# Performance work log

Measured on AMD Instinct MI355X. Metric: run time of the kernel, lower is better.

## Reference

```python
import jax, jax.numpy as jnp
import numpy as np
from jax import lax

FH, FW = 14, 14
HID = 1024

def _coord():
    idx = np.arange(FH * FW)
    c = np.stack([(idx / FW - FH // 2) / (FH / 2.0), (idx % FW - FW // 2) / (FW / 2.0)], axis=1)
    # view(1,H,W,2) -> transpose(2,3) -> transpose(1,2) == (1,2,H,W)
    return jnp.asarray(c.reshape(1, FH, FW, 2).transpose(0, 3, 1, 2), jnp.float32)

def _l2n(x, axis):
    # F.normalize: x / max(||x||_2, 1e-12)
    return x / jnp.maximum(jnp.linalg.norm(x, axis=axis, keepdims=True), 1e-12)

def _conv(x, w, b, pad):
    y = lax.conv_general_dilated(x, w, (1, 1), [(pad, pad), (pad, pad)],
                                 dimension_numbers=('NCHW', 'OIHW', 'NCHW'))
    return y + b[None, :, None, None]

def _bn(x, g, b):
    # BatchNorm2d in training mode: batch statistics, eps=1e-5
    m = jnp.mean(x, (0, 2, 3), keepdims=True)
    v = jnp.var(x, (0, 2, 3), keepdims=True)
    return g[None, :, None, None] * (x - m) * lax.rsqrt(v + 1e-5) + b[None, :, None, None]

def _lstm(x, w_ih, w_hh, b_ih, b_hh):
    # x: [S,B,E]; PyTorch gate order i,f,g,o
    B = x.shape[1]
    h0 = jnp.zeros((B, HID), x.dtype)
    def step(carry, xt):
        h, c = carry
        g = xt @ w_ih.T + h @ w_hh.T + (b_ih + b_hh)
        i, f, gg, o = jnp.split(g, 4, axis=-1)
        c = jax.nn.sigmoid(f) * c + jax.nn.sigmoid(i) * jnp.tanh(gg)
        h = jax.nn.sigmoid(o) * jnp.tanh(c)
        return (h, c), h
    _, hs = lax.scan(step, (h0, h0), x)
    return hs  # [S,B,HID]

def _res(v, coord, c1w, c1b, c2w, c2b, g, b):
    v = jnp.concatenate([v, coord], 1)            # [B,130,14,14]
    v1 = jax.nn.relu(_conv(v, c1w, c1b, 0))        # 1x1 conv
    v2 = jax.nn.relu(_bn(_conv(v1, c2w, c2b, 1), g, b))
    return v2 + v1

def _forward(que, img, emb_table, w_ih_f, w_hh_f, b_ih_f, b_hh_f, w_ih_b, w_hh_b, b_ih_b, b_hh_b,
             conv_w, conv_b, bn_g, bn_b, r1c1_w, r1c1_b, r1c2_w, r1c2_b, r1bn_g, r1bn_b,
             r2c1_w, r2c1_b, r2c2_w, r2c2_b, r2bn_g, r2bn_b):
    emb_table = emb_table.at[0].set(0.0)  # padding_idx=0
    x = jnp.swapaxes(emb_table[que], 0, 1)                 # [S,B,300]
    hf = _lstm(x, w_ih_f, w_hh_f, b_ih_f, b_hh_f)
    hb = _lstm(x[::-1], w_ih_b, w_hh_b, b_ih_b, b_hh_b)[::-1]
    qenc = _l2n(jnp.concatenate([hf, hb], -1), -1)         # [S,B,2048]
    enc = qenc[-1]                                         # [B,2048]
    v = _l2n(img, 1)                                       # L2 norm over channels per pixel
    B = img.shape[0]
    coord = jnp.broadcast_to(_coord(), (B, 2, FH, FW))
    v = jnp.concatenate([v, coord], 1)                     # [B,1026,14,14]
    v = jax.nn.relu(_bn(_conv(v, conv_w, conv_b, 1), bn_g, bn_b))
    v = _res(v, coord, r1c1_w, r1c1_b, r1c2_w, r1c2_b, r1bn_g, r1bn_b)
    v = _res(v, coord, r2c1_w, r2c1_b, r2c2_w, r2c2_b, r2bn_g, r2bn_b)
    return enc, qenc, v

def setup_inputs():
    key = jax.random.key(0)
    ks = jax.random.split(key, 32)
    B, S, V = 128, 32, 10000
    def n(k, shape, s=0.03):
        return jax.random.normal(k, shape, jnp.float32) * s
    return {
        'que': jax.random.randint(ks[0], (B, S), 0, V + 1),
        'img': jax.random.normal(ks[1], (B, 1024, FH, FW), jnp.float32),
        'emb_table': n(ks[2], (V + 1, 300), 0.1),
        'w_ih_f': n(ks[3], (4 * HID, 300)), 'w_hh_f': n(ks[4], (4 * HID, HID)),
        'b_ih_f': n(ks[5], (4 * HID,)), 'b_hh_f': n(ks[6], (4 * HID,)),
        'w_ih_b': n(ks[7], (4 * HID, 300)), 'w_hh_b': n(ks[8], (4 * HID, HID)),
        'b_ih_b': n(ks[9], (4 * HID,)), 'b_hh_b': n(ks[10], (4 * HID,)),
        'conv_w': n(ks[11], (128, 1026, 3, 3)), 'conv_b': n(ks[12], (128,)),
        'bn_g': jnp.ones((128,), jnp.float32), 'bn_b': jnp.zeros((128,), jnp.float32),
        'r1c1_w': n(ks[13], (128, 130, 1, 1)), 'r1c1_b': n(ks[14], (128,)),
        'r1c2_w': n(ks[15], (128, 128, 3, 3)), 'r1c2_b': n(ks[16], (128,)),
        'r1bn_g': jnp.ones((128,), jnp.float32), 'r1bn_b': jnp.zeros((128,), jnp.float32),
        'r2c1_w': n(ks[17], (128, 130, 1, 1)), 'r2c1_b': n(ks[18], (128,)),
        'r2c2_w': n(ks[19], (128, 128, 3, 3)), 'r2c2_b': n(ks[20], (128,)),
        'r2bn_g': jnp.ones((128,), jnp.float32), 'r2bn_b': jnp.zeros((128,), jnp.float32),
    }

def reference(que, img, emb_table, w_ih_f, w_hh_f, b_ih_f, b_hh_f, w_ih_b, w_hh_b, b_ih_b, b_hh_b,
              conv_w, conv_b, bn_g, bn_b, r1c1_w, r1c1_b, r1c2_w, r1c2_b, r1bn_g, r1bn_b,
              r2c1_w, r2c1_b, r2c2_w, r2c2_b, r2bn_g, r2bn_b):
    return _forward(que, img, emb_table, w_ih_f, w_hh_f, b_ih_f, b_hh_f, w_ih_b, w_hh_b, b_ih_b, b_hh_b,
                    conv_w, conv_b, bn_g, bn_b, r1c1_w, r1c1_b, r1c2_w, r1c2_b, r1bn_g, r1bn_b,
                    r2c1_w, r2c1_b, r2c2_w, r2c2_b, r2bn_g, r2bn_b)
```

## Files before the change

### kernel.cpp

```cpp
#include <hip/hip_runtime.h>
#include <hip/hip_bf16.h>
#include <math.h>


namespace {

constexpr int S_ = 32, B_ = 128, H_ = 1024, P_ = 196, OC_ = 128;
constexpr int NE = B_ * OC_ * P_;
constexpr int KC = 44;

typedef __attribute__((ext_vector_type(8))) short short8v;
typedef __attribute__((ext_vector_type(4))) short short4v;
typedef __attribute__((ext_vector_type(4))) float f32x4;
#define MFMA16(a, b, c) __builtin_amdgcn_mfma_f32_16x16x32_bf16((a), (b), (c), 0, 0, 0)

__device__ __forceinline__ float sigm(float x){ return 1.0f/(1.0f + expf(-x)); }
__device__ __forceinline__ float c0f(int p){ return ((float)p/14.0f - 7.0f)/7.0f; }
__device__ __forceinline__ float c1f(int p){ return ((float)(p%14) - 7.0f)/7.0f; }
__device__ __forceinline__ unsigned short f2bf(float x){
  __hip_bfloat16 h = __float2bfloat16(x);
  return *reinterpret_cast<unsigned short*>(&h);
}
__device__ __forceinline__ float bf2f(unsigned short u){
  unsigned v = ((unsigned)u) << 16;
  union { unsigned u; float f; } c; c.u = v; return c.f;
}

__global__ void k_packW2(const float* __restrict__ wihf, const float* __restrict__ whhf,
                         const float* __restrict__ wihb, const float* __restrict__ whhb,
                         unsigned short* __restrict__ pk){
  int i = blockIdx.x*256 + threadIdx.x;
  if (i >= 2*32*4*2*KC*64) return;
  const int lane = i & 63;
  int t = i >> 6;
  const int kc = t % KC; t /= KC;
  const int pair = t % 2; t /= 2;
  const int w = t % 4; t /= 4;
  const int uslab = t % 32; t /= 32;
  const int dir = t;
  const int lr = lane & 15, lk = lane >> 4;
  const int row = (pair*2 + (lr >> 3))*1024 + uslab*32 + w*8 + (lr & 7);
  unsigned short v[8];
  if (kc < 12){
    const float* src = dir ? wihb : wihf;
    #pragma unroll
    for (int j = 0; j < 8; ++j){
      int k = kc*32 + lk*8 + j;
      v[j] = (k < 300) ? f2bf(src[(size_t)row*300 + k]) : (unsigned short)0;
    }
  } else {
    const float* src = dir ? whhb : whhf;
    #pragma unroll
    for (int j = 0; j < 8; ++j)
      v[j] = f2bf(src[(size_t)row*1024 + (kc-12)*32 + lk*8 + j]);
  }
  unsigned short* dst = pk + (size_t)i*8;
  #pragma unroll
  for (int j = 0; j < 8; ++j) dst[j] = v[j];
}

__global__ void k_embed_px(const int* __restrict__ que, const float* __restrict__ emb,
                           unsigned short* __restrict__ px){
  int i = blockIdx.x*256 + threadIdx.x;
  if (i >= 32*8*12*64) return;
  const int lane = i & 63;
  int t2 = i >> 6;
  const int kc = t2 % 12; t2 /= 12;
  const int mgrp = t2 % 8; t2 /= 8;
  const int t = t2;
  const int b = mgrp*16 + (lane & 15);
  const int tok = que[b*S_ + t];
  const int k0 = kc*32 + (lane >> 4)*8;
  unsigned short* dst = px + (size_t)i*8;
  #pragma unroll
  for (int j = 0; j < 8; ++j){
    int k = k0 + j;
    dst[j] = (tok == 0 || k >= 300) ? (unsigned short)0 : f2bf(emb[(size_t)tok*300 + k]);
  }
}

__launch_bounds__(256, 4)
__global__ void k_xg(const unsigned short* __restrict__ px,
                     const unsigned short* __restrict__ pkW2,
                     unsigned short* __restrict__ xg){
  const int dir = blockIdx.x >> 5, uslab = blockIdx.x & 31;
  const int mslab = blockIdx.y;
  const int xs = blockIdx.z;
  const int tid = threadIdx.x, w = tid >> 6, lane = tid & 63;

  const unsigned short* pb = pkW2 + ((((size_t)(dir*32 + uslab)*4 + w)*2)*KC*64 + lane)*8;
  const size_t pbPair = (size_t)KC*512;
  const unsigned short* pax = px + (((size_t)(xs*8 + mslab*2)*12)*64 + lane)*8;
  const size_t paxRf = (size_t)12*512;

  f32x4 a00{0,0,0,0}, a01{0,0,0,0}, a10{0,0,0,0}, a11{0,0,0,0};
  #pragma unroll 4
  for (int ch = 0; ch < 12; ++ch){
    short8v a0 = *(const short8v*)(pax + (size_t)ch*512);
    short8v a1 = *(const short8v*)(pax + paxRf + (size_t)ch*512);
    short8v b0 = *(const short8v*)(pb + (size_t)ch*512);
    short8v b1 = *(const short8v*)(pb + pbPair + (size_t)ch*512);
    a00 = MFMA16(a0, b0, a00); a01 = MFMA16(a0, b1, a01);
    a10 = MFMA16(a1, b0, a10); a11 = MFMA16(a1, b1, a11);
  }

  const size_t rid = (((size_t)((xs*2 + dir)*4 + mslab)*32 + uslab)*4 + w);
  unsigned short* rec = xg + rid*1024;
  f32x4 accs[4] = {a00, a01, a10, a11};
  #pragma unroll
  for (int r = 0; r < 2; ++r)
    #pragma unroll
    for (int p = 0; p < 2; ++p){
      f32x4 v = accs[r*2 + p];
      short4v sv;
      #pragma unroll
      for (int j = 0; j < 4; ++j) sv[j] = (short)f2bf(v[j]);
      *(short4v*)(rec + ((p*2 + r)*64 + lane)*4) = sv;
    }
}

__global__ void k_packC(const float* __restrict__ w, unsigned short* __restrict__ pk,
                        int cin, int T){
  int i = blockIdx.x*256 + threadIdx.x;
  if (i >= 9*8*T*64) return;
  const int lane = i & 63;
  int t = i >> 6;
  const int kc = t % T; t /= T;
  const int ot = t % 8; t /= 8;
  const int s = t;
  const int oc = ot*16 + (lane & 15);
  const int c0 = kc*32 + (lane >> 4)*8;
  unsigned short* dst = pk + (((size_t)(s*8 + ot)*T + kc)*64 + lane)*8;
  #pragma unroll
  for (int j = 0; j < 8; ++j){
    int c = c0 + j;
    dst[j] = (c < cin) ? f2bf(w[((size_t)oc*cin + c)*9 + s]) : (unsigned short)0;
  }
}

__global__ void k_packG(const float* __restrict__ w, unsigned short* __restrict__ pk,
                        int cin, int T){
  int i = blockIdx.x*256 + threadIdx.x;
  if (i >= 8*T*64) return;
  const int lane = i & 63;
  int t = i >> 6;
  const int kc = t % T; t /= T;
  const int ot = t;
  const int oc = ot*16 + (lane & 15);
  const int c0 = kc*32 + (lane >> 4)*8;
  unsigned short* dst = pk + (((size_t)(ot*T + kc))*64 + lane)*8;
  #pragma unroll
  for (int j = 0; j < 8; ++j){
    int c = c0 + j;
    dst[j] = (c < cin) ? f2bf(w[(size_t)oc*cin + c]) : (unsigned short)0;
  }
}

__global__ void k_bias2(const float* __restrict__ bif, const float* __restrict__ bhf,
                        const float* __restrict__ bib, const float* __restrict__ bhb,
                        float* __restrict__ out){
  int i = blockIdx.x*256 + threadIdx.x;
  if (i >= 8192) return;
  out[i] = (i < 4096) ? (bif[i] + bhf[i]) : (bib[i-4096] + bhb[i-4096]);
}

__global__ void k_coordT(unsigned short* __restrict__ outT){
  int i = blockIdx.x*256 + threadIdx.x;
  if (i >= 128*196*32) return;
  int c2 = i & 31; int t = i >> 5; int p = t % 196; int b = t / 196;
  float v = (c2 == 0) ? c0f(p) : (c2 == 1) ? c1f(p) : 0.f;
  outT[((size_t)b*196 + p)*160 + 128 + c2] = f2bf(v);
}

__launch_bounds__(256, 2)
__global__ void k_step10(const unsigned short* __restrict__ xg,
                         const unsigned short* __restrict__ pkW2,
                         const float* __restrict__ bias2,
                         const unsigned short* __restrict__ hin,
                         unsigned short* __restrict__ hout,
                         float* __restrict__ cst, float* __restrict__ Q, int s){
  const int dir   = blockIdx.x >> 5;
  const int uslab = blockIdx.x & 31;
  const int mslab = blockIdx.y;
  const int m0g   = mslab*32;
  const int tid = threadIdx.x, w = tid >> 6, lane = tid & 63;
  const int lr = lane & 15, lk = lane >> 4;
  const int xs = dir ? (S_-1-s) : s;

  __shared__ unsigned short tA[32][1032];

  {
    const int r = tid >> 3, sg = tid & 7;
    const unsigned short* hr = hin + ((size_t)dir*B_ + m0g + r)*H_ + sg*128;
    #pragma unroll
    for (int q = 0; q < 16; ++q)
      *(short8v*)&tA[r][sg*128 + q*8] = *(const short8v*)(hr + q*8);
  }

  const size_t rid = (((size_t)((xs*2 + dir)*4 + mslab)*32 + uslab)*4 + w);
  const unsigned short* rec = xg + rid*1024;
  f32x4 a00, a01, a10, a11;
  {
    short4v s00 = *(const short4v*)(rec + ((0*2 + 0)*64 + lane)*4);
    short4v s01 = *(const short4v*)(rec + ((1*2 + 0)*64 + lane)*4);
    short4v s10 = *(const short4v*)(rec + ((0*2 + 1)*64 + lane)*4);
    short4v s11 = *(const short4v*)(rec + ((1*2 + 1)*64 + lane)*4);
    #pragma unroll
    for (int j = 0; j < 4; ++j){
      a00[j] = bf2f((unsigned short)s00[j]);
      a01[j] = bf2f((unsigned short)s01[j]);
      a10[j] = bf2f((unsigned short)s10[j]);
      a11[j] = bf2f((unsigned short)s11[j]);
    }
  }

  const unsigned short* pb = pkW2 + ((((size_t)(dir*32 + uslab)*4 + w)*2)*KC*64 + lane)*8;
  const size_t pbPair = (size_t)KC*512;

  __syncthreads();

  #pragma unroll 8
  for (int ch = 0; ch < 32; ++ch){
    const int ka = ch*32 + lk*8;
    short8v a0 = *(short8v*)&tA[lr][ka];
    short8v a1 = *(short8v*)&tA[16 + lr][ka];
    short8v b0 = *(const short8v*)(pb + (size_t)(12 + ch)*512);
    short8v b1 = *(const short8v*)(pb + pbPair + (size_t)(12 + ch)*512);
    a00 = MFMA16(a0, b0, a00); a01 = MFMA16(a0, b1, a01);
    a10 = MFMA16(a1, b0, a10); a11 = MFMA16(a1, b1, a11);
  }

  const int ug = uslab*32 + w*8 + (lr & 7);
  const float* bb = bias2 + (size_t)dir*4096;
  const float bi = bb[ug], bfv = bb[1024+ug], bg = bb[2048+ug], bo = bb[3072+ug];
  float* cc = cst + (size_t)dir*B_*H_;
  unsigned short* ho = hout + (size_t)dir*B_*H_;
  const int jbase = (lr & 8) ? 2 : 0;

  #pragma unroll
  for (int rf = 0; rf < 2; ++rf){
    f32x4 c0 = rf ? a10 : a00;
    f32x4 c1 = rf ? a11 : a01;
    float p0[4], p1[4];
    #pragma unroll
    for (int j = 0; j < 4; ++j){
      p0[j] = __shfl_xor(c0[j], 8, 64);
      p1[j] = __shfl_xor(c1[j], 8, 64);
    }
    #pragma unroll
    for (int q = 0; q < 2; ++q){
      const int jj = jbase + q;
      float gi, gf, gg, go;
      if (lr & 8){ gi = p0[jj]; gf = c0[jj]; gg = p1[jj]; go = c1[jj]; }
      else       { gi = c0[jj]; gf = p0[jj]; gg = c1[jj]; go = p1[jj]; }
      gi += bi; gf += bfv; gg += bg; go += bo;
      const int m = m0g + rf*16 + lk*4 + jj;
      const size_t coff = (size_t)m*H_ + ug;
      float cold = cc[coff];
      float cn = sigm(gf)*cold + sigm(gi)*tanhf(gg);
      float hn = sigm(go)*tanhf(cn);
      cc[coff] = cn;
      ho[coff] = f2bf(hn);
      Q[((size_t)xs*B_ + m)*2048 + dir*1024 + ug] = hn;
    }
  }
}

__global__ void k_qnorm(float* __restrict__ Q, float* __restrict__ enc){
  int sb = blockIdx.x;
  int s = sb >> 7, b = sb & 127;
  float* row = Q + (size_t)sb*2048;
  int tid = threadIdx.x;
  float v[8]; float ss = 0.f;
  #pragma unroll
  for (int i = 0; i < 8; ++i){ v[i] = row[tid*8+i]; ss += v[i]*v[i]; }
  __shared__ float red[256];
  red[tid] = ss; __syncthreads();
  for (int st = 128; st; st >>= 1){
    if (tid < st) red[tid] += red[tid+st];
    __syncthreads();
  }
  float inv = 1.0f / fmaxf(sqrtf(red[0]), 1e-12f);
  #pragma unroll
  for (int i = 0; i < 8; ++i){
    float q = v[i]*inv;
    row[tid*8+i] = q;
    if (s == S_-1) enc[(size_t)b*2048 + tid*8 + i] = q;
  }
}

__global__ void k_sqpart(const float* __restrict__ img, float* __restrict__ part){
  int b = blockIdx.x, cq = blockIdx.y;
  int t = threadIdx.x;
  if (t >= P_) return;
  const float* base = img + ((size_t)b*1024 + cq*256)*P_ + t;
  float s = 0.f;
  #pragma unroll 4
  for (int c = 0; c < 256; ++c){ float v = base[c*P_]; s += v*v; }
  part[((size_t)b*4 + cq)*P_ + t] = s;
}

__global__ void k_invnorm(const float* __restrict__ part, float* __restrict__ inv){
  int i = blockIdx.x*256 + threadIdx.x;
  if (i >= B_*P_) return;
  int b = i / P_, p = i % P_;
  float s = part[(b*4+0)*P_+p] + part[(b*4+1)*P_+p]
          + part[(b*4+2)*P_+p] + part[(b*4+3)*P_+p];
  inv[i] = 1.0f / fmaxf(sqrtf(s), 1e-12f);
}

__global__ void k_mkimgT(const float* __restrict__ img, const float* __restrict__ invn,
                         unsigned short* __restrict__ imgT){
  const int b = blockIdx.x, cg = blockIdx.y;
  const int tid = threadIdx.x;
  unsigned short* dstB = imgT + (size_t)b*196*1056;
  if (cg == 8){
    for (int i = tid; i < 196*32; i += 256){
      int p = i >> 5, cc = i & 31;
      float v = (cc == 0) ? c0f(p) : (cc == 1) ? c1f(p) : 0.f;
      dstB[(size_t)p*1056 + 1024 + cc] = f2bf(v);
    }
    return;
  }
  __shared__ unsigned short tt[196][136];
  __shared__ float sInv[200];
  for (int i = tid; i < 196; i += 256) sInv[i] = invn[b*196 + i];
  __syncthreads();
  const int c0 = cg*128;
  const float* srcB = img + ((size_t)b*1024 + c0)*196;
  for (int i = tid; i < 128*49; i += 256){
    int c = i / 49, p4 = i - (i/49)*49;
    float4 v = *(const float4*)(srcB + (size_t)c*196 + p4*4);
    int p = p4*4;
    tt[p+0][c] = f2bf(v.x * sInv[p+0]);
    tt[p+1][c] = f2bf(v.y * sInv[p+1]);
    tt[p+2][c] = f2bf(v.z * sInv[p+2]);
    tt[p+3][c] = f2bf(v.w * sInv[p+3]);
  }
  __syncthreads();
  for (int i = tid; i < 196*16; i += 256){
    int p = i >> 4, g = i & 15;
    *(short8v*)(dstB + (size_t)p*1056 + c0 + g*8) = *(short8v*)&tt[p][g*8];
  }
}

template<int CPAD>
__device__ __forceinline__ void stage3t(unsigned short (*__restrict__ tile)[40],
                                        const unsigned short* __restrict__ src,
                                        int c0, int r0, int tid){
  for (int i = tid; i < 10*14*4; i += 256){
    int t = i / 56, rem = i - t*56, gx = rem >> 2, seg = rem & 3;
    int gy = r0 - 1 + t;
    if ((unsigned)gy < 14u){
      short8v v = *(const short8v*)(src + (size_t)(gy*14+gx)*CPAD + c0 + seg*8);
      *(short8v*)&tile[t*16 + gx + 1][seg*8] = v;
    }
  }
}

template<int CPAD>
__launch_bounds__(256, 2)
__global__ void k_conv3t(const unsigned short* __restrict__ srcT,
                         const unsigned short* __restrict__ wPk,
                         const float* __restrict__ bias,
                         float* __restrict__ out){
  constexpr int T = CPAD / 32;
  const int b = blockIdx.x, n = blockIdx.y, z = blockIdx.z;
  const int r0 = n ? 6 : 0;
  const int chBeg = z ? T/2 : 0, chEnd = z ? T : T/2;
  const int tid = threadIdx.x, wave = tid >> 6, lane = tid & 63;
  const int lr = lane & 15, lk = lane >> 4;
  const int wfM = wave >> 1, wfN = wave & 1;
  const unsigned short* src = srcT + (size_t)b*196*CPAD;

  __shared__ unsigned short tile[2][164][40];

  for (int i = tid; i < 1640; i += 256)
    ((short8v*)&tile[0][0][0])[i] = short8v{0,0,0,0,0,0,0,0};
  __syncthreads();
  stage3t<CPAD>(tile[0], src, chBeg*32, r0, tid);
  __syncthreads();

  f32x4 acc[4][4];
  #pragma unroll
  for (int i = 0; i < 4; ++i)
    #pragma unroll
    for (int j = 0; j < 4; ++j) acc[i][j] = f32x4{0,0,0,0};

  short8v aC[12], aN[12];
  #pragma unroll
  for (int dx = 0; dx < 3; ++dx)
    #pragma unroll
    for (int rf = 0; rf < 4; ++rf)
      aC[dx*4+rf] = *(const short8v*)(wPk + ((((size_t)dx*8 + wfM*4 + rf)*T + chBeg)*64
                                             + lane)*8);

  for (int ch = chBeg; ch < chEnd; ++ch){
    const int cur = (ch - chBeg) & 1;
    #pragma unroll
    for (int dy = 0; dy < 3; ++dy){
      const int ndy = (dy < 2) ? dy + 1 : 0;
      const int nch = (dy < 2) ? ch : ch + 1;
      const bool hasN = nch < chEnd;
      if (hasN){
        #pragma unroll
        for (int dx = 0; dx < 3; ++dx)
          #pragma unroll
          for (int rf = 0; rf < 4; ++rf)
            aN[dx*4+rf] = *(const short8v*)(wPk + ((((size_t)(ndy*3+dx)*8 + wfM*4 + rf)*T
                                                    + nch)*64 + lane)*8);
      }
      #pragma unroll
      for (int dx = 0; dx < 3; ++dx){
        const int dlt = dy*16 + dx;
        #pragma unroll
        for (int cf = 0; cf < 4; ++cf){
          short8v bf = *(short8v*)&tile[cur][wfN*64 + cf*16 + lr + dlt][lk*8];
          #pragma unroll
          for (int rf = 0; rf < 4; ++rf)
            acc[rf][cf] = MFMA16(aC[dx*4+rf], bf, acc[rf][cf]);
        }
      }
      if (dy == 0 && ch + 1 < chEnd)
        stage3t<CPAD>(tile[cur^1], src, (ch+1)*32, r0, tid);
      if (hasN){
        #pragma unroll
        for (int q = 0; q < 12; ++q) aC[q] = aN[q];
      }
    }
    __syncthreads();
  }

  #pragma unroll
  for (int rf = 0; rf < 4; ++rf){
    #pragma unroll
    for (int j = 0; j < 4; ++j){
      const int oc = wfM*64 + rf*16 + lk*4 + j;
      const float bz = z ? 0.f : bias[oc];
      #pragma unroll
      for (int cf = 0; cf < 4; ++cf){
        const int pos = wfN*64 + cf*16 + lr;
        const int py = r0 + (pos >> 4), px = pos & 15;
        const bool rowok = n ? (py >= 8) : true;
        if (rowok && px < 14)
          out[(size_t)z*NE + ((size_t)b*OC_ + oc)*P_ + py*14 + px] = acc[rf][cf][j] + bz;
      }
    }
  }
}

__global__ void k_bnstats2(const float* __restrict__ t, float* __restrict__ bpart){
  const int o = blockIdx.x, part = blockIdx.y;
  const int tid = threadIdx.x;
  float s = 0.f, s2 = 0.f;
  for (int i = tid; i < 16*196; i += 256){
    int b = part*16 + i/196, p = i - (i/196)*196;
    size_t off = ((size_t)b*OC_ + o)*P_ + p;
    float v = t[off] + t[off + NE];
    s += v; s2 += v*v;
  }
  __shared__ float r1[256], r2[256];
  r1[tid] = s; r2[tid] = s2; __syncthreads();
  for (int st = 128; st; st >>= 1){
    if (tid < st){ r1[tid] += r1[tid+st]; r2[tid] += r2[tid+st]; }
    __syncthreads();
  }
  if (tid == 0){
    bpart[(o*8 + part)*2]     = r1[0];
    bpart[(o*8 + part)*2 + 1] = r2[0];
  }
}

__global__ void k_bnfin(const float* __restrict__ bpart, float* __restrict__ stats){
  int o = threadIdx.x;
  if (o >= 128) return;
  float s = 0.f, s2 = 0.f;
  #pragma unroll
  for (int q = 0; q < 8; ++q){
    s  += bpart[(o*8 + q)*2];
    s2 += bpart[(o*8 + q)*2 + 1];
  }
  float n = (float)(B_*P_);
  float m = s / n;
  float var = s2 / n - m*m;
  stats[o*2]   = m;
  stats[o*2+1] = rsqrtf(var + 1e-5f);
}

template<bool ADD, bool FINAL>
__global__ void k_bntr(const float* __restrict__ t, const float* __restrict__ stats,
                       const float* __restrict__ g, const float* __restrict__ bb,
                       const float* __restrict__ addsrc,
                       float* __restrict__ outF, unsigned short* __restrict__ outT){
  const int b = blockIdx.x, seg = blockIdx.y, tid = threadIdx.x;
  for (int i = tid; i < 16*196; i += 256){
    int c = seg*16 + i/196, p = i - (i/196)*196;
    size_t off = ((size_t)b*OC_ + c)*P_ + p;
    float x = t[off] + t[off + NE];
    float v = g[c]*(x - stats[c*2])*stats[c*2+1] + bb[c];
    v = fmaxf(v, 0.f);
    if (ADD) v += addsrc[off];
    if (FINAL) outF[off] = v;
    else       outT[((size_t)b*P_ + p)*160 + c] = f2bf(v);
  }
}

__launch_bounds__(256, 2)
__global__ void k_c1m(const unsigned short* __restrict__ vT,
                      const unsigned short* __restrict__ pk,
                      const float* __restrict__ bias,
                      float* __restrict__ out, unsigned short* __restrict__ outT){
  const int b = blockIdx.x, n = blockIdx.y;
  const int pBeg = n ? 112 : 0;
  const int nCF = n ? 6 : 7;
  const int tid = threadIdx.x, wave = tid >> 6, lane = tid & 63;
  const int lr = lane & 15, lk = lane >> 4;

  __shared__ unsigned short tile[112][164];

  for (int i = tid; i < 112*20; i += 256){
    int r = i / 20, seg = i - r*20;
    int p = pBeg + r;
    short8v v = short8v{0,0,0,0,0,0,0,0};
    if (p < 196 && r < nCF*16)
      v = *(const short8v*)(vT + ((size_t)b*P_ + p)*160 + seg*8);
    *(short8v*)&tile[r][seg*8] = v;
  }
  __syncthreads();

  f32x4 acc[2][7];
  #pragma unroll
  for (int i = 0; i < 2; ++i)
    #pragma unroll
    for (int j = 0; j < 7; ++j) acc[i][j] = f32x4{0,0,0,0};

  #pragma unroll
  for (int kc = 0; kc < 5; ++kc){
    short8v a0 = *(const short8v*)(pk + (((size_t)(wave*2 + 0)*5 + kc)*64 + lane)*8);
    short8v a1 = *(const short8v*)(pk + (((size_t)(wave*2 + 1)*5 + kc)*64 + lane)*8);
    #pragma unroll
    for (int cf = 0; cf < 7; ++cf){
      if (cf < nCF){
        short8v bf = *(short8v*)&tile[cf*16 + lr][kc*32 + lk*8];
        acc[0][cf] = MFMA16(a0, bf, acc[0][cf]);
        acc[1][cf] = MFMA16(a1, bf, acc[1][cf]);
      }
    }
  }

  #pragma unroll
  for (int rf = 0; rf < 2; ++rf){
    const int ocBase = wave*32 + rf*16 + lk*4;
    #pragma unroll
    for (int cf = 0; cf < 7; ++cf){
      if (cf < nCF){
        const int pos = pBeg + cf*16 + lr;
        if (pos < 196){
          short4v sv;
          #pragma unroll
          for (int j = 0; j < 4; ++j){
            const int oc = ocBase + j;
            float v = fmaxf(acc[rf][cf][j] + bias[oc], 0.f);
            out[((size_t)b*OC_ + oc)*P_ + pos] = v;
            sv[j] = (short)f2bf(v);
          }
          *(short4v*)(outT + ((size_t)b*P_ + pos)*128 + ocBase) = sv;
        }
      }
    }
  }
}

}

extern "C" void kernel_launch(void* const* d_in, const int* in_sizes, int n_in,
                              void* d_out, int out_size, void* d_ws, size_t ws_size,
                              hipStream_t stream){
  (void)in_sizes; (void)n_in; (void)out_size; (void)ws_size;
  const int*   que  = (const int*)  d_in[0];
  const float* img  = (const float*)d_in[1];
  const float* emb  = (const float*)d_in[2];
  const float* wihf = (const float*)d_in[3];
  const float* whhf = (const float*)d_in[4];
  const float* bihf = (const float*)d_in[5];
  const float* bhhf = (const float*)d_in[6];
  const float* wihb = (const float*)d_in[7];
  const float* whhb = (const float*)d_in[8];
  const float* bihb = (const float*)d_in[9];
  const float* bhhb = (const float*)d_in[10];
  const float* convw = (const float*)d_in[11];
  const float* convb = (const float*)d_in[12];
  const float* bng  = (const float*)d_in[13];
  const float* bnb  = (const float*)d_in[14];
  const float* r1c1w = (const float*)d_in[15];
  const float* r1c1b = (const float*)d_in[16];
  const float* r1c2w = (const float*)d_in[17];
  const float* r1c2b = (const float*)d_in[18];
  const float* r1bng = (const float*)d_in[19];
  const float* r1bnb = (const float*)d_in[20];
  const float* r2c1w = (const float*)d_in[21];
  const float* r2c1b = (const float*)d_in[22];
  const float* r2c2w = (const float*)d_in[23];
  const float* r2c2b = (const float*)d_in[24];
  const float* r2bng = (const float*)d_in[25];
  const float* r2bnb = (const float*)d_in[26];

  float* out  = (float*)d_out;
  float* enc  = out;
  float* Q    = out + 262144;
  float* vout = out + 262144 + 8388608;

  float* ws = (float*)d_ws;
  unsigned short* px   = (unsigned short*)ws;
  unsigned short* pkW2 = (unsigned short*)(ws + 786432);
  float* bias2 = ws + 6553600;
  unsigned short* hstate = (unsigned short*)(ws + 6561792);
  float* cstate = ws + 6823936;
  float* part   = ws + 7086080;
  float* invn   = ws + 7186432;
  float* stats  = ws + 7211520;
  float* bpart  = ws + 7211776;
  unsigned short* pkC  = (unsigned short*)(ws + 7213824);
  unsigned short* pkR1 = (unsigned short*)(ws + 7822080);
  unsigned short* pkR2 = (unsigned short*)(ws + 7895808);
  unsigned short* pk1  = (unsigned short*)(ws + 7969536);
  unsigned short* pk2  = (unsigned short*)(ws + 7979776);
  float* U = ws + 7990016;
  unsigned short* xg = (unsigned short*)U;
  float* bufB = U;
  float* convOut = U + NE;
  unsigned short* imgT = (unsigned short*)(U + 3*(size_t)NE);
  unsigned short* vTb  = (unsigned short*)(U + 9633792 + 13246464);
  unsigned short* v1T  = (unsigned short*)(U + 9633792 + 13246464 + 2007040);

  hipMemsetAsync(hstate, 0, (size_t)(262144 + 262144)*sizeof(float), stream);

  k_packW2<<<(2*32*4*2*KC*64 + 255)/256, 256, 0, stream>>>(wihf, whhf, wihb, whhb, pkW2);
  k_embed_px<<<(32*8*12*64 + 255)/256, 256, 0, stream>>>(que, emb, px);
  k_packC<<<(9*8*33*64 + 255)/256, 256, 0, stream>>>(convw, pkC, 1026, 33);
  k_packC<<<(9*8*4*64 + 255)/256, 256, 0, stream>>>(r1c2w, pkR1, 128, 4);
  k_packC<<<(9*8*4*64 + 255)/256, 256, 0, stream>>>(r2c2w, pkR2, 128, 4);
  k_packG<<<(8*5*64 + 255)/256, 256, 0, stream>>>(r1c1w, pk1, 130, 5);
  k_packG<<<(8*5*64 + 255)/256, 256, 0, stream>>>(r2c1w, pk2, 130, 5);
  k_bias2<<<32, 256, 0, stream>>>(bihf, bhhf, bihb, bhhb, bias2);
  k_coordT<<<(128*196*32 + 255)/256, 256, 0, stream>>>(vTb);

  k_xg<<<dim3(64,4,32), 256, 0, stream>>>(px, pkW2, xg);

  for (int s = 0; s < 32; ++s){
    unsigned short* hin  = hstate + (size_t)(s & 1)*262144;
    unsigned short* hout = hstate + (size_t)((s & 1)^1)*262144;
    k_step10<<<dim3(64,4), 256, 0, stream>>>(xg, pkW2, bias2, hin, hout,
                                             cstate, Q, s);
  }
  k_qnorm<<<4096, 256, 0, stream>>>(Q, enc);

  k_sqpart<<<dim3(128,4), 256, 0, stream>>>(img, part);
  k_invnorm<<<(25088+255)/256, 256, 0, stream>>>(part, invn);
  k_mkimgT<<<dim3(128,9), 256, 0, stream>>>(img, invn, imgT);

  k_conv3t<1056><<<dim3(128,2,2), 256, 0, stream>>>(imgT, pkC, convb, convOut);
  k_bnstats2<<<dim3(128,8), 256, 0, stream>>>(convOut, bpart);
  k_bnfin<<<1, 128, 0, stream>>>(bpart, stats);
  k_bntr<false,false><<<dim3(128,8), 256, 0, stream>>>(convOut, stats, bng, bnb,
                                                       nullptr, nullptr, vTb);

  k_c1m<<<dim3(128,2), 256, 0, stream>>>(vTb, pk1, r1c1b, bufB, v1T);
  k_conv3t<128><<<dim3(128,2,2), 256, 0, stream>>>(v1T, pkR1, r1c2b, convOut);
  k_bnstats2<<<dim3(128,8), 256, 0, stream>>>(convOut, bpart);
  k_bnfin<<<1, 128, 0, stream>>>(bpart, stats);
  k_bntr<true,false><<<dim3(128,8), 256, 0, stream>>>(convOut, stats, r1bng, r1bnb,
                                                      bufB, nullptr, vTb);

  k_c1m<<<dim3(128,2), 256, 0, stream>>>(vTb, pk2, r2c1b, bufB, v1T);
  k_conv3t<128><<<dim3(128,2,2), 256, 0, stream>>>(v1T, pkR2, r2c2b, convOut);
  k_bnstats2<<<dim3(128,8), 256, 0, stream>>>(convOut, bpart);
  k_bnfin<<<1, 128, 0, stream>>>(bpart, stats);
  k_bntr<true,true><<<dim3(128,8), 256, 0, stream>>>(convOut, stats, r2bng, r2bnb,
                                                     bufB, vout, nullptr);
}
```

Before: 833.8 us.

## Halve LSTM step row tile and split 3x3 convs four ways along K

The recurrent LSTM step kernel now gives each block 16 batch rows instead of 32, which doubles the grid to 512 blocks and raises the launch-bounds occupancy target. Each block drops to two MFMA accumulators, and the step's precomputed input-gate half-tile is chosen by mslab parity. The three 3x3 conv kernels split their input channels four ways instead of two, so the BN stats and transform kernels now sum four partial outputs, and the workspace offsets move to make room. The aim is more parallelism in the latency-bound serial LSTM steps and in the convs. The cost is reading the recurrent weights twice as many times per step, plus extra partial-sum traffic for the convs.

```diff
diff --git a/kernel.cpp b/kernel.cpp
--- a/kernel.cpp
+++ b/kernel.cpp
@@ -172,8 +172,8 @@
   outT[((size_t)b*196 + p)*160 + 128 + c2] = f2bf(v);
 }
 
-__launch_bounds__(256, 2)
-__global__ void k_step10(const unsigned short* __restrict__ xg,
+__launch_bounds__(256, 4)
+__global__ void k_step11(const unsigned short* __restrict__ xg,
                          const unsigned short* __restrict__ pkW2,
                          const float* __restrict__ bias2,
                          const unsigned short* __restrict__ hin,
@@ -182,35 +182,34 @@
   const int dir   = blockIdx.x >> 5;
   const int uslab = blockIdx.x & 31;
   const int mslab = blockIdx.y;
-  const int m0g   = mslab*32;
+  const int m0g   = mslab*16;
   const int tid = threadIdx.x, w = tid >> 6, lane = tid & 63;
   const int lr = lane & 15, lk = lane >> 4;
   const int xs = dir ? (S_-1-s) : s;
 
-  __shared__ unsigned short tA[32][1032];
+  __shared__ unsigned short tA[16][1032];
 
   {
-    const int r = tid >> 3, sg = tid & 7;
-    const unsigned short* hr = hin + ((size_t)dir*B_ + m0g + r)*H_ + sg*128;
-    #pragma unroll
-    for (int q = 0; q < 16; ++q)
-      *(short8v*)&tA[r][sg*128 + q*8] = *(const short8v*)(hr + q*8);
-  }
-
-  const size_t rid = (((size_t)((xs*2 + dir)*4 + mslab)*32 + uslab)*4 + w);
+    const int r = tid >> 4, sg = tid & 15;
+    const unsigned short* hr = hin + ((size_t)dir*B_ + m0g + r)*H_;
+    #pragma unroll
+    for (int q = 0; q < 8; ++q){
+      const int u = sg + q*16;
+      *(short8v*)&tA[r][u*8] = *(const short8v*)(hr + u*8);
+    }
+  }
+
+  const size_t rid = (((size_t)((xs*2 + dir)*4 + (mslab >> 1))*32 + uslab)*4 + w);
+  const int rf = mslab & 1;
   const unsigned short* rec = xg + rid*1024;
-  f32x4 a00, a01, a10, a11;
+  f32x4 a00, a01;
   {
-    short4v s00 = *(const short4v*)(rec + ((0*2 + 0)*64 + lane)*4);
-    short4v s01 = *(const short4v*)(rec + ((1*2 + 0)*64 + lane)*4);
-    short4v s10 = *(const short4v*)(rec + ((0*2 + 1)*64 + lane)*4);
-    short4v s11 = *(const short4v*)(rec + ((1*2 + 1)*64 + lane)*4);
+    short4v s0 = *(const short4v*)(rec + ((0*2 + rf)*64 + lane)*4);
+    short4v s1 = *(const short4v*)(rec + ((1*2 + rf)*64 + lane)*4);
     #pragma unroll
     for (int j = 0; j < 4; ++j){
-      a00[j] = bf2f((unsigned short)s00[j]);
-      a01[j] = bf2f((unsigned short)s01[j]);
-      a10[j] = bf2f((unsigned short)s10[j]);
-      a11[j] = bf2f((unsigned short)s11[j]);
+      a00[j] = bf2f((unsigned short)s0[j]);
+      a01[j] = bf2f((unsigned short)s1[j]);
     }
   }
 
@@ -223,11 +222,10 @@
   for (int ch = 0; ch < 32; ++ch){
     const int ka = ch*32 + lk*8;
     short8v a0 = *(short8v*)&tA[lr][ka];
-    short8v a1 = *(short8v*)&tA[16 + lr][ka];
     short8v b0 = *(const short8v*)(pb + (size_t)(12 + ch)*512);
     short8v b1 = *(const short8v*)(pb + pbPair + (size_t)(12 + ch)*512);
-    a00 = MFMA16(a0, b0, a00); a01 = MFMA16(a0, b1, a01);
-    a10 = MFMA16(a1, b0, a10); a11 = MFMA16(a1, b1, a11);
+    a00 = MFMA16(a0, b0, a00);
+    a01 = MFMA16(a0, b1, a01);
   }
 
   const int ug = uslab*32 + w*8 + (lr & 7);
@@ -237,32 +235,27 @@
   unsigned short* ho = hout + (size_t)dir*B_*H_;
   const int jbase = (lr & 8) ? 2 : 0;
 
-  #pragma unroll
-  for (int rf = 0; rf < 2; ++rf){
-    f32x4 c0 = rf ? a10 : a00;
-    f32x4 c1 = rf ? a11 : a01;
-    float p0[4], p1[4];
-    #pragma unroll
-    for (int j = 0; j < 4; ++j){
-      p0[j] = __shfl_xor(c0[j], 8, 64);
-      p1[j] = __shfl_xor(c1[j], 8, 64);
-    }
-    #pragma unroll
-    for (int q = 0; q < 2; ++q){
-      const int jj = jbase + q;
-      float gi, gf, gg, go;
-      if (lr & 8){ gi = p0[jj]; gf = c0[jj]; gg = p1[jj]; go = c1[jj]; }
-      else       { gi = c0[jj]; gf = p0[jj]; gg = c1[jj]; go = p1[jj]; }
-      gi += bi; gf += bfv; gg += bg; go += bo;
-      const int m = m0g + rf*16 + lk*4 + jj;
-      const size_t coff = (size_t)m*H_ + ug;
-      float cold = cc[coff];
-      float cn = sigm(gf)*cold + sigm(gi)*tanhf(gg);
-      float hn = sigm(go)*tanhf(cn);
-      cc[coff] = cn;
-      ho[coff] = f2bf(hn);
-      Q[((size_t)xs*B_ + m)*2048 + dir*1024 + ug] = hn;
-    }
+  float p0[4], p1[4];
+  #pragma unroll
+  for (int j = 0; j < 4; ++j){
+    p0[j] = __shfl_xor(a00[j], 8, 64);
+    p1[j] = __shfl_xor(a01[j], 8, 64);
+  }
+  #pragma unroll
+  for (int q = 0; q < 2; ++q){
+    const int jj = jbase + q;
+    float gi, gf, gg, go;
+    if (lr & 8){ gi = p0[jj]; gf = a00[jj]; gg = p1[jj]; go = a01[jj]; }
+    else       { gi = a00[jj]; gf = p0[jj]; gg = a01[jj]; go = p1[jj]; }
+    gi += bi; gf += bfv; gg += bg; go += bo;
+    const int m = m0g + lk*4 + jj;
+    const size_t coff = (size_t)m*H_ + ug;
+    float cold = cc[coff];
+    float cn = sigm(gf)*cold + sigm(gi)*tanhf(gg);
+    float hn = sigm(go)*tanhf(cn);
+    cc[coff] = cn;
+    ho[coff] = f2bf(hn);
+    Q[((size_t)xs*B_ + m)*2048 + dir*1024 + ug] = hn;
   }
 }
 
@@ -359,7 +352,7 @@
 }
 
 template<int CPAD>
-__launch_bounds__(256, 2)
+__launch_bounds__(256, 4)
 __global__ void k_conv3t(const unsigned short* __restrict__ srcT,
                          const unsigned short* __restrict__ wPk,
                          const float* __restrict__ bias,
@@ -367,7 +360,7 @@
   constexpr int T = CPAD / 32;
   const int b = blockIdx.x, n = blockIdx.y, z = blockIdx.z;
   const int r0 = n ? 6 : 0;
-  const int chBeg = z ? T/2 : 0, chEnd = z ? T : T/2;
+  const int chBeg = (z*T)/4, chEnd = ((z+1)*T)/4;
   const int tid = threadIdx.x, wave = tid >> 6, lane = tid & 63;
   const int lr = lane & 15, lk = lane >> 4;
   const int wfM = wave >> 1, wfN = wave & 1;
@@ -456,7 +449,7 @@
   for (int i = tid; i < 16*196; i += 256){
     int b = part*16 + i/196, p = i - (i/196)*196;
     size_t off = ((size_t)b*OC_ + o)*P_ + p;
-    float v = t[off] + t[off + NE];
+    float v = t[off] + t[off + NE] + t[off + 2*(size_t)NE] + t[off + 3*(size_t)NE];
     s += v; s2 += v*v;
   }
   __shared__ float r1[256], r2[256];
@@ -496,7 +489,7 @@
   for (int i = tid; i < 16*196; i += 256){
     int c = seg*16 + i/196, p = i - (i/196)*196;
     size_t off = ((size_t)b*OC_ + c)*P_ + p;
-    float x = t[off] + t[off + NE];
+    float x = t[off] + t[off + NE] + t[off + 2*(size_t)NE] + t[off + 3*(size_t)NE];
     float v = g[c]*(x - stats[c*2])*stats[c*2+1] + bb[c];
     v = fmaxf(v, 0.f);
     if (ADD) v += addsrc[off];
@@ -629,9 +622,9 @@
   unsigned short* xg = (unsigned short*)U;
   float* bufB = U;
   float* convOut = U + NE;
-  unsigned short* imgT = (unsigned short*)(U + 3*(size_t)NE);
-  unsigned short* vTb  = (unsigned short*)(U + 9633792 + 13246464);
-  unsigned short* v1T  = (unsigned short*)(U + 9633792 + 13246464 + 2007040);
+  unsigned short* imgT = (unsigned short*)(U + 5*(size_t)NE);
+  unsigned short* vTb  = (unsigned short*)(U + 5*(size_t)NE + 13246464);
+  unsigned short* v1T  = (unsigned short*)(U + 5*(size_t)NE + 13246464 + 2007040);
 
   hipMemsetAsync(hstate, 0, (size_t)(262144 + 262144)*sizeof(float), stream);
 
@@ -650,7 +643,7 @@
   for (int s = 0; s < 32; ++s){
     unsigned short* hin  = hstate + (size_t)(s & 1)*262144;
     unsigned short* hout = hstate + (size_t)((s & 1)^1)*262144;
-    k_step10<<<dim3(64,4), 256, 0, stream>>>(xg, pkW2, bias2, hin, hout,
+    k_step11<<<dim3(64,8), 256, 0, stream>>>(xg, pkW2, bias2, hin, hout,
                                              cstate, Q, s);
   }
   k_qnorm<<<4096, 256, 0, stream>>>(Q, enc);
@@ -659,21 +652,21 @@
   k_invnorm<<<(25088+255)/256, 256, 0, stream>>>(part, invn);
   k_mkimgT<<<dim3(128,9), 256, 0, stream>>>(img, invn, imgT);
 
-  k_conv3t<1056><<<dim3(128,2,2), 256, 0, stream>>>(imgT, pkC, convb, convOut);
+  k_conv3t<1056><<<dim3(128,2,4), 256, 0, stream>>>(imgT, pkC, convb, convOut);
   k_bnstats2<<<dim3(128,8), 256, 0, stream>>>(convOut, bpart);
   k_bnfin<<<1, 128, 0, stream>>>(bpart, stats);
   k_bntr<false,false><<<dim3(128,8), 256, 0, stream>>>(convOut, stats, bng, bnb,
                                                        nullptr, nullptr, vTb);
 
   k_c1m<<<dim3(128,2), 256, 0, stream>>>(vTb, pk1, r1c1b, bufB, v1T);
-  k_conv3t<128><<<dim3(128,2,2), 256, 0, stream>>>(v1T, pkR1, r1c2b, convOut);
+  k_conv3t<128><<<dim3(128,2,4), 256, 0, stream>>>(v1T, pkR1, r1c2b, convOut);
   k_bnstats2<<<dim3(128,8), 256, 0, stream>>>(convOut, bpart);
   k_bnfin<<<1, 128, 0, stream>>>(bpart, stats);
   k_bntr<true,false><<<dim3(128,8), 256, 0, stream>>>(convOut, stats, r1bng, r1bnb,
                                                       bufB, nullptr, vTb);
 
   k_c1m<<<dim3(128,2), 256, 0, stream>>>(vTb, pk2, r2c1b, bufB, v1T);
-  k_conv3t<128><<<dim3(128,2,2), 256, 0, stream>>>(v1T, pkR2, r2c2b, convOut);
+  k_conv3t<128><<<dim3(128,2,4), 256, 0, stream>>>(v1T, pkR2, r2c2b, convOut);
   k_bnstats2<<<dim3(128,8), 256, 0, stream>>>(convOut, bpart);
   k_bnfin<<<1, 128, 0, stream>>>(bpart, stats);
   k_bntr<true,true><<<dim3(128,8), 256, 0, stream>>>(convOut, stats, r2bng, r2bnb,
```

After: 1.480 ms. 1.77x slower.
